# Optimization experiments

Measured on AMD Instinct MI355X. Metric: run time of the kernel, lower is better.

The kernel has to match this reference:

```python
import jax, jax.numpy as jnp
import numpy as np

WIN = 8          # current_window
PRETRAIN = 8     # pretrain_window
HEADS = 8
SHIFT = WIN // 2 # shift_size, shift_dir = [1, 1] (shift_mode=1)
L = WIN * WIN
LOG100 = float(np.log(100.0))


def _shift_mask(H, W):
    # bands (shift_dir=[1,1], no padding). Pairs from different regions get -100.
    hr = np.repeat(np.arange(3), [H - WIN, WIN - SHIFT, SHIFT])
    wr = np.repeat(np.arange(3), [W - WIN, WIN - SHIFT, SHIFT])
    region = hr[:, None] * 3 + wr[None, :]                      # [H, W]
    reg = region.reshape(H // WIN, WIN, W // WIN, WIN)
    reg = reg.transpose(0, 2, 1, 3).reshape(-1, L)              # [nw, L]
    m = np.where(reg[:, :, None] != reg[:, None, :], -100.0, 0.0)
    return jnp.asarray(m, dtype=jnp.float32)[None, :, None]     # [1, nw, 1, L, L]


def _rel_bias(cpb_w1, cpb_b1, cpb_w2):
    # Swin-v2 continuous relative position bias (log-spaced coords + MLP).
    pos = np.stack(np.meshgrid(np.arange(WIN), np.arange(WIN), indexing='ij'), -1).reshape(L, 2)
    rc = (pos[:, None, :] - pos[None, :, :]).astype(np.float32)  # [L, L, 2]
    rc = rc / (PRETRAIN - 1) * 8.0
    rc = np.sign(rc) * np.log2(np.abs(rc) + 1.0) / np.log2(8.0)
    rc = jnp.asarray(rc)
    bias = jax.nn.relu(rc @ cpb_w1 + cpb_b1) @ cpb_w2            # [L, L, heads]
    bias = 16.0 * jax.nn.sigmoid(bias)
    return bias.transpose(2, 0, 1)                               # [heads, L, L]


def _l2n(a):
    # tf.math.l2_normalize with epsilon=1.55e-5
    return a * jax.lax.rsqrt(jnp.maximum(jnp.sum(a * a, -1, keepdims=True), 1.55e-5))


def setup_inputs() -> dict:
    key = jax.random.key(0)
    ks = jax.random.split(key, 6)
    B, H, W, C = 16, 128, 128, 256
    cpb = 512
    return {
        'x': jax.random.normal(ks[0], (B, H, W, C), jnp.float32),
        'qkv_w': jax.random.normal(ks[1], (C, 3 * C), jnp.float32) * 0.02,
        'q_bias': jnp.zeros((C,), jnp.float32),
        'v_bias': jnp.zeros((C,), jnp.float32),
        'scale': jnp.full((HEADS, 1, 1), np.log(10.0), jnp.float32),
        'cpb_w1': jax.random.normal(ks[2], (2, cpb), jnp.float32) * 0.02,
        'cpb_b1': jnp.zeros((cpb,), jnp.float32),
        'cpb_w2': jax.random.normal(ks[3], (cpb, HEADS), jnp.float32) * 0.02,
        'proj_w': jax.random.normal(ks[4], (C, C), jnp.float32) * 0.02,
        'proj_b': jnp.zeros((C,), jnp.float32),
    }


def reference(x, qkv_w, q_bias, v_bias, scale, cpb_w1, cpb_b1, cpb_w2, proj_w, proj_b):
    B, H, W, C = x.shape
    units = C // HEADS
    # qkv 1x1 conv + (q, 0, v) bias
    bias = jnp.concatenate([q_bias, jnp.zeros_like(q_bias), v_bias])
    qkv = jnp.einsum('bhwc,cd->bhwd', x, qkv_w) + bias
    # cyclic shift (H, W > window so shift is applied; no padding needed)
    qkv = jnp.roll(qkv, (-SHIFT, -SHIFT), axis=(1, 2))
    # fused window partition -> [B, nw, heads, L, 3*units]
    nh, nw = H // WIN, W // WIN
    t = qkv.reshape(B, nh, WIN, nw, WIN, HEADS, 3 * units)
    t = t.transpose(0, 1, 3, 5, 2, 4, 6).reshape(B, nh * nw, HEADS, L, 3 * units)
    q, k, v = jnp.split(t, 3, axis=-1)
    # cosine attention with clamped learned logit scale
    logit_scale = jnp.exp(jnp.minimum(scale, LOG100))            # [heads, 1, 1]
    attn = jnp.einsum('bnhld,bnhmd->bnhlm', _l2n(q) * logit_scale, _l2n(k))
    attn = attn + _rel_bias(cpb_w1, cpb_b1, cpb_w2)[None, None] + _shift_mask(H, W)
    attn = jax.nn.softmax(attn, axis=-1)
    out = jnp.einsum('bnhlm,bnhmd->bnhld', attn, v)
    # reverse partition, reverse shift, output projection
    out = out.reshape(B, nh, nw, HEADS, WIN, WIN, units)
    out = out.transpose(0, 1, 4, 2, 5, 3, 6).reshape(B, H, W, C)
    out = jnp.roll(out, (SHIFT, SHIFT), axis=(1, 2))
    return jnp.einsum('bhwc,cd->bhwd', out, proj_w) + proj_b
```

## Files before the change

kernel.cpp:

```cpp
#include <hip/hip_runtime.h>

typedef __attribute__((ext_vector_type(4))) float  f32x4;
typedef __attribute__((ext_vector_type(8))) __bf16 bf16x8;
typedef __attribute__((ext_vector_type(4))) __bf16 bf16x4;

__global__ __launch_bounds__(256) void wprep_kernel(const float* __restrict__ qw,
                                                    const float* __restrict__ pw,
                                                    const float* __restrict__ qb,
                                                    const float* __restrict__ vb,
                                                    __bf16* __restrict__ W2,
                                                    __bf16* __restrict__ pT,
                                                    float* __restrict__ bcat) {
  int i = blockIdx.x * 256 + threadIdx.x;
  if (i < 24576) {
    int h = i / 3072, rem = i - h * 3072;
    int ft = rem >> 9, rem2 = rem & 511;
    int ks = rem2 >> 6, l = rem2 & 63;
    int g = l >> 4, c = l & 15;
    int col = h * 96 + ft * 16 + c;
    bf16x8 v;
    #pragma unroll
    for (int j = 0; j < 8; ++j)
      v[j] = (__bf16)qw[(ks * 32 + g * 8 + j) * 768 + col];
    *(bf16x8*)(W2 + (size_t)i * 8) = v;
  } else if (i < 24576 + 65536) {
    int j = i - 24576;
    int n = j >> 8, k = j & 255;
    pT[j] = (__bf16)pw[k * 256 + n];
  } else if (i < 24576 + 65536 + 768) {
    int cdx = i - 24576 - 65536;
    bcat[cdx] = (cdx < 256) ? qb[cdx] : ((cdx < 512) ? 0.0f : vb[cdx - 512]);
  }
}

__global__ __launch_bounds__(256) void cpb_kernel(const float* __restrict__ w1,
                                                  const float* __restrict__ b1,
                                                  const float* __restrict__ w2,
                                                  float* __restrict__ bias) {
  int pair = blockIdx.x * 256 + threadIdx.x;
  int lq = pair >> 6, mk = pair & 63;
  float d0 = (float)((lq >> 3) - (mk >> 3));
  float d1 = (float)((lq & 7) - (mk & 7));
  float v0 = d0 * (8.0f / 7.0f);
  float v1 = d1 * (8.0f / 7.0f);
  float s0 = (v0 > 0.f) ? 1.f : ((v0 < 0.f) ? -1.f : 0.f);
  float s1 = (v1 > 0.f) ? 1.f : ((v1 < 0.f) ? -1.f : 0.f);
  float r0 = s0 * log2f(fabsf(v0) + 1.0f) * (1.0f / 3.0f);
  float r1 = s1 * log2f(fabsf(v1) + 1.0f) * (1.0f / 3.0f);
  float acc[8] = {0.f, 0.f, 0.f, 0.f, 0.f, 0.f, 0.f, 0.f};
  #pragma unroll 4
  for (int j = 0; j < 512; ++j) {
    float h = fmaxf(r0 * w1[j] + r1 * w1[512 + j] + b1[j], 0.0f);
    #pragma unroll
    for (int q = 0; q < 8; ++q) acc[q] += h * w2[j * 8 + q];
  }
  #pragma unroll
  for (int q = 0; q < 8; ++q) {
    float s = 16.0f / (1.0f + __expf(-acc[q]));
    bias[(q * 64 + lq) * 64 + mk] = s;
  }
}

__device__ __forceinline__ int win_region(int tok, int wi, int wj) {
  int r = tok >> 3, cc = tok & 7;
  int rh = (wi == 15) ? ((r < 4) ? 1 : 2) : 0;
  int rw = (wj == 15) ? ((cc < 4) ? 1 : 2) : 0;
  return rh * 3 + rw;
}

__global__ __launch_bounds__(512, 2) void fused_kernel(
    const float* __restrict__ x, const __bf16* __restrict__ W2,
    const float* __restrict__ bcat, const float* __restrict__ scale,
    const float* __restrict__ cpb, __bf16* __restrict__ out)
{
  __shared__ __align__(16) __bf16 xs[64 * 256];
  __shared__ __align__(16) __bf16 qkp[8][64 * 72];
  __shared__ __align__(16) __bf16 vst[8][64 * 36];
  const f32x4 zz = {0.f, 0.f, 0.f, 0.f};

  int t = threadIdx.x;
  int h = t >> 6, l = t & 63, g = l >> 4, c = l & 15;
  int win = blockIdx.x, b = blockIdx.y;
  int wi = win >> 4, wj = win & 15;
  bool edge = (wi == 15) || (wj == 15);

  {
    int r = t >> 3;
    int q8 = t & 7;
    int ht = (wi * 8 + (r >> 3) + 4) & 127;
    int wt = (wj * 8 + (r & 7) + 4) & 127;
    const float* src = x + (size_t)((b * 128 + ht) * 128 + wt) * 256 + q8 * 32;
    #pragma unroll
    for (int q = 0; q < 4; ++q) {
      f32x4 a0 = *(const f32x4*)(src + q * 8);
      f32x4 a1 = *(const f32x4*)(src + q * 8 + 4);
      bf16x8 v;
      #pragma unroll
      for (int j = 0; j < 4; ++j) { v[j] = (__bf16)a0[j]; v[4 + j] = (__bf16)a1[j]; }
      int phys = (q8 * 4 + q) ^ (r & 7);
      *(bf16x8*)&xs[r * 256 + phys * 8] = v;
    }
  }
  __syncthreads();

  int toko[4];
  #pragma unroll
  for (int i = 0; i < 4; ++i) {
    int tok = 16 * i + c;
    int ht = (wi * 8 + (tok >> 3) + 4) & 127;
    int wt = (wj * 8 + (tok & 7) + 4) & 127;
    toko[i] = ((b * 128 + ht) * 128 + wt) * 256;
  }

  f32x4 acc[6][4];
  #pragma unroll
  for (int ft = 0; ft < 6; ++ft)
    #pragma unroll
    for (int tt = 0; tt < 4; ++tt) acc[ft][tt] = zz;

  const __bf16* Wh = W2 + (size_t)h * 24576;
  #pragma unroll
  for (int ks = 0; ks < 8; ++ks) {
    bf16x8 wf[6], xf[4];
    #pragma unroll
    for (int ft = 0; ft < 6; ++ft)
      wf[ft] = *(const bf16x8*)(Wh + (size_t)((ft * 8 + ks) * 64 + l) * 8);
    #pragma unroll
    for (int tt = 0; tt < 4; ++tt) {
      int phys = (ks * 4 + g) ^ (c & 7);
      xf[tt] = *(const bf16x8*)&xs[(tt * 16 + c) * 256 + phys * 8];
    }
    #pragma unroll
    for (int ft = 0; ft < 6; ++ft)
      #pragma unroll
      for (int tt = 0; tt < 4; ++tt)
        acc[ft][tt] = __builtin_amdgcn_mfma_f32_16x16x32_bf16(wf[ft], xf[tt], acc[ft][tt], 0, 0, 0);
  }

  #pragma unroll
  for (int ft = 0; ft < 6; ++ft) {
    f32x4 bb = *(const f32x4*)&bcat[h * 96 + ft * 16 + 4 * g];
    #pragma unroll
    for (int tt = 0; tt < 4; ++tt) acc[ft][tt] += bb;
  }

  float ls = __expf(fminf(scale[h], 4.6051701859880914f));

  #pragma unroll
  for (int tt = 0; tt < 4; ++tt) {
    float sq = 0.f, sk = 0.f;
    #pragma unroll
    for (int i = 0; i < 4; ++i) {
      sq += acc[0][tt][i] * acc[0][tt][i] + acc[1][tt][i] * acc[1][tt][i];
      sk += acc[2][tt][i] * acc[2][tt][i] + acc[3][tt][i] * acc[3][tt][i];
    }
    sq += __shfl_xor(sq, 16); sq += __shfl_xor(sq, 32);
    sk += __shfl_xor(sk, 16); sk += __shfl_xor(sk, 32);
    float rq = rsqrtf(fmaxf(sq, 1.55e-5f)) * ls;
    float rk = rsqrtf(fmaxf(sk, 1.55e-5f));
    __bf16* row = &qkp[h][(tt * 16 + c) * 72];
    bf16x4 w0, w1, w2, w3, v0, v1;
    #pragma unroll
    for (int i = 0; i < 4; ++i) {
      w0[i] = (__bf16)(acc[0][tt][i] * rq);
      w1[i] = (__bf16)(acc[1][tt][i] * rq);
      w2[i] = (__bf16)(acc[2][tt][i] * rk);
      w3[i] = (__bf16)(acc[3][tt][i] * rk);
      v0[i] = (__bf16)acc[4][tt][i];
      v1[i] = (__bf16)acc[5][tt][i];
    }
    *(bf16x4*)&row[4 * g]      = w0;
    *(bf16x4*)&row[16 + 4 * g] = w1;
    *(bf16x4*)&row[32 + 4 * g] = w2;
    *(bf16x4*)&row[48 + 4 * g] = w3;
    __bf16* vrow = &vst[h][(tt * 16 + c) * 36];
    *(bf16x4*)&vrow[4 * g]      = v0;
    *(bf16x4*)&vrow[16 + 4 * g] = v1;
  }

  bf16x8 kf[4], qf[4];
  #pragma unroll
  for (int i = 0; i < 4; ++i) {
    kf[i] = *(const bf16x8*)&qkp[h][(16 * i + c) * 72 + 32 + 8 * g];
    qf[i] = *(const bf16x8*)&qkp[h][(16 * i + c) * 72 + 8 * g];
  }

  float rsum[4];
  __bf16* Pw = &qkp[h][0];
  #pragma unroll
  for (int nt = 0; nt < 4; ++nt) {
    f32x4 tt4[4];
    #pragma unroll
    for (int mt = 0; mt < 4; ++mt)
      tt4[mt] = __builtin_amdgcn_mfma_f32_16x16x32_bf16(kf[mt], qf[nt], zz, 0, 0, 0);
    int q = nt * 16 + c;
    float p[16];
    #pragma unroll
    for (int mt = 0; mt < 4; ++mt) {
      f32x4 bb = *(const f32x4*)&cpb[(h * 64 + q) * 64 + mt * 16 + 4 * g];
      #pragma unroll
      for (int i = 0; i < 4; ++i) p[mt * 4 + i] = tt4[mt][i] + bb[i];
    }
    if (edge) {
      int regq = win_region(q, wi, wj);
      #pragma unroll
      for (int mt = 0; mt < 4; ++mt)
        #pragma unroll
        for (int i = 0; i < 4; ++i) {
          int k = mt * 16 + 4 * g + i;
          if (win_region(k, wi, wj) != regq) p[mt * 4 + i] -= 100.0f;
        }
    }
    float mx = -1e30f;
    #pragma unroll
    for (int j = 0; j < 16; ++j) mx = fmaxf(mx, p[j]);
    mx = fmaxf(mx, __shfl_xor(mx, 16));
    mx = fmaxf(mx, __shfl_xor(mx, 32));
    float sum = 0.f;
    #pragma unroll
    for (int j = 0; j < 16; ++j) { p[j] = __expf(p[j] - mx); sum += p[j]; }
    sum += __shfl_xor(sum, 16); sum += __shfl_xor(sum, 32);
    rsum[nt] = sum;
    #pragma unroll
    for (int mt = 0; mt < 4; ++mt) {
      bf16x4 px = { (__bf16)p[mt * 4 + 0], (__bf16)p[mt * 4 + 1],
                    (__bf16)p[mt * 4 + 2], (__bf16)p[mt * 4 + 3] };
      *(bf16x4*)&Pw[q * 72 + mt * 16 + 4 * g] = px;
    }
  }

  #pragma unroll
  for (int mh = 0; mh < 2; ++mh) {
    f32x4 oacc[4];
    #pragma unroll
    for (int nt = 0; nt < 4; ++nt) oacc[nt] = zz;
    #pragma unroll
    for (int ks = 0; ks < 2; ++ks) {
      bf16x8 va;
      #pragma unroll
      for (int j = 0; j < 8; ++j)
        va[j] = vst[h][(32 * ks + 8 * g + j) * 36 + 16 * mh + c];
      #pragma unroll
      for (int nt = 0; nt < 4; ++nt) {
        bf16x8 pfr = *(const bf16x8*)&Pw[(nt * 16 + c) * 72 + 32 * ks + 8 * g];
        oacc[nt] = __builtin_amdgcn_mfma_f32_16x16x32_bf16(va, pfr, oacc[nt], 0, 0, 0);
      }
    }
    #pragma unroll
    for (int nt = 0; nt < 4; ++nt) {
      float rinv = 1.0f / rsum[nt];
      bf16x4 ov = { (__bf16)(oacc[nt][0] * rinv), (__bf16)(oacc[nt][1] * rinv),
                    (__bf16)(oacc[nt][2] * rinv), (__bf16)(oacc[nt][3] * rinv) };
      *(bf16x4*)(out + toko[nt] + h * 32 + 16 * mh + 4 * g) = ov;
    }
  }
}

__global__ __launch_bounds__(256) void proj_kernel(
    const __bf16* __restrict__ A, const __bf16* __restrict__ BT,
    float* __restrict__ Cout, const float* __restrict__ pb)
{
  const int K = 256, N = 256, NB = 2;
  __shared__ __align__(16) __bf16 lA[128 * 64];
  __shared__ __align__(16) __bf16 lB[128 * 64];
  int t = threadIdx.x;
  int wv = t >> 6, l = t & 63;
  int g = l >> 4, c = l & 15;
  int wr = wv >> 1, wc = wv & 1;

  int cpx = gridDim.x >> 3;
  int lin = (blockIdx.x & 7) * cpx + (blockIdx.x >> 3);
  int mblk = lin / NB;
  int nblk = lin - mblk * NB;

  int srow = wv * 8 + (l >> 3);
  const __bf16* Ab = A + (size_t)mblk * 128 * K;
  const __bf16* Bb = BT + (size_t)nblk * 128 * K;

  f32x4 acc[4][4];
  #pragma unroll
  for (int i = 0; i < 4; ++i)
    #pragma unroll
    for (int j = 0; j < 4; ++j) acc[i][j] = (f32x4){0.f, 0.f, 0.f, 0.f};

  for (int kt = 0; kt < 4; ++kt) {
    bf16x8 ra[4], rb[4];
    #pragma unroll
    for (int p = 0; p < 4; ++p) {
      ra[p] = *(const bf16x8*)(Ab + (size_t)(p * 32 + srow) * K + kt * 64 + (l & 7) * 8);
      rb[p] = *(const bf16x8*)(Bb + (size_t)(p * 32 + srow) * K + kt * 64 + (l & 7) * 8);
    }
    __syncthreads();
    #pragma unroll
    for (int p = 0; p < 4; ++p) {
      int row = p * 32 + srow;
      int phys = (l & 7) ^ (row & 7);
      *(bf16x8*)&lA[row * 64 + phys * 8] = ra[p];
      *(bf16x8*)&lB[row * 64 + phys * 8] = rb[p];
    }
    __syncthreads();
    #pragma unroll
    for (int kk = 0; kk < 2; ++kk) {
      bf16x8 af[4], bfr[4];
      #pragma unroll
      for (int mt = 0; mt < 4; ++mt) {
        int row = wr * 64 + mt * 16 + c;
        int ch = ((kk << 2) | g) ^ (c & 7);
        af[mt] = *(const bf16x8*)&lA[row * 64 + ch * 8];
      }
      #pragma unroll
      for (int nt = 0; nt < 4; ++nt) {
        int row = wc * 64 + nt * 16 + c;
        int ch = ((kk << 2) | g) ^ (c & 7);
        bfr[nt] = *(const bf16x8*)&lB[row * 64 + ch * 8];
      }
      #pragma unroll
      for (int mt = 0; mt < 4; ++mt)
        #pragma unroll
        for (int nt = 0; nt < 4; ++nt)
          acc[mt][nt] = __builtin_amdgcn_mfma_f32_16x16x32_bf16(af[mt], bfr[nt], acc[mt][nt], 0, 0, 0);
    }
  }

  #pragma unroll
  for (int mt = 0; mt < 4; ++mt) {
    #pragma unroll
    for (int nt = 0; nt < 4; ++nt) {
      int row0 = mblk * 128 + wr * 64 + mt * 16 + 4 * g;
      int col  = nblk * 128 + wc * 64 + nt * 16 + c;
      float bias = pb[col];
      #pragma unroll
      for (int i = 0; i < 4; ++i)
        Cout[(size_t)(row0 + i) * N + col] = acc[mt][nt][i] + bias;
    }
  }
}

extern "C" void kernel_launch(void* const* d_in, const int* in_sizes, int n_in,
                              void* d_out, int out_size, void* d_ws, size_t ws_size,
                              hipStream_t stream)
{
  const float* x      = (const float*)d_in[0];
  const float* qkv_w  = (const float*)d_in[1];
  const float* q_bias = (const float*)d_in[2];
  const float* v_bias = (const float*)d_in[3];
  const float* scale  = (const float*)d_in[4];
  const float* cpb_w1 = (const float*)d_in[5];
  const float* cpb_b1 = (const float*)d_in[6];
  const float* cpb_w2 = (const float*)d_in[7];
  const float* proj_w = (const float*)d_in[8];
  const float* proj_b = (const float*)d_in[9];

  char* ws = (char*)d_ws;
  __bf16* aout = (__bf16*)(ws);
  __bf16* W2   = (__bf16*)(ws + 134217728LL);
  __bf16* pT   = (__bf16*)(ws + 134610944LL);
  float*  bcat = (float*) (ws + 134742016LL);
  float*  cpb  = (float*) (ws + 134745088LL);

  wprep_kernel<<<355, 256, 0, stream>>>(qkv_w, proj_w, q_bias, v_bias, W2, pT, bcat);
  cpb_kernel<<<16, 256, 0, stream>>>(cpb_w1, cpb_b1, cpb_w2, cpb);
  fused_kernel<<<dim3(256, 16), 512, 0, stream>>>(x, W2, bcat, scale, cpb, aout);
  proj_kernel<<<4096, 256, 0, stream>>>(aout, pT, (float*)d_out, proj_b);
}
```

Before: 407.0 us.

## Fuse output projection into windowed attention kernel via shared-memory staging

Removes the separate projection GEMM kernel. Each block writes its attention output back into the xs shared buffer with a swizzled layout, then every wave computes a 32-column slice of the output projection with MFMA and writes fp32 results straight to the destination. This drops the 128 MB bf16 intermediate round trip through global memory and one kernel launch. It adds extra MFMA work and more register pressure to the already heavy fused kernel, plus an extra barrier.

```diff
diff --git a/kernel.cpp b/kernel.cpp
--- a/kernel.cpp
+++ b/kernel.cpp
@@ -9,7 +9,7 @@
                                                     const float* __restrict__ qb,
                                                     const float* __restrict__ vb,
                                                     __bf16* __restrict__ W2,
-                                                    __bf16* __restrict__ pT,
+                                                    __bf16* __restrict__ Wp,
                                                     float* __restrict__ bcat) {
   int i = blockIdx.x * 256 + threadIdx.x;
   if (i < 24576) {
@@ -23,12 +23,20 @@
     for (int j = 0; j < 8; ++j)
       v[j] = (__bf16)qw[(ks * 32 + g * 8 + j) * 768 + col];
     *(bf16x8*)(W2 + (size_t)i * 8) = v;
-  } else if (i < 24576 + 65536) {
+  } else if (i < 24576 + 8192) {
     int j = i - 24576;
-    int n = j >> 8, k = j & 255;
-    pT[j] = (__bf16)pw[k * 256 + n];
-  } else if (i < 24576 + 65536 + 768) {
-    int cdx = i - 24576 - 65536;
+    int wv = j >> 10, rem = j & 1023;
+    int ft = rem >> 9, rem2 = rem & 511;
+    int ks = rem2 >> 6, l = rem2 & 63;
+    int g = l >> 4, c = l & 15;
+    int col = wv * 32 + ft * 16 + c;
+    bf16x8 v;
+    #pragma unroll
+    for (int j8 = 0; j8 < 8; ++j8)
+      v[j8] = (__bf16)pw[(ks * 32 + g * 8 + j8) * 256 + col];
+    *(bf16x8*)(Wp + (size_t)j * 8) = v;
+  } else if (i < 24576 + 8192 + 768) {
+    int cdx = i - 24576 - 8192;
     bcat[cdx] = (cdx < 256) ? qb[cdx] : ((cdx < 512) ? 0.0f : vb[cdx - 512]);
   }
 }
@@ -70,8 +78,9 @@
 
 __global__ __launch_bounds__(512, 2) void fused_kernel(
     const float* __restrict__ x, const __bf16* __restrict__ W2,
-    const float* __restrict__ bcat, const float* __restrict__ scale,
-    const float* __restrict__ cpb, __bf16* __restrict__ out)
+    const __bf16* __restrict__ Wp, const float* __restrict__ bcat,
+    const float* __restrict__ scale, const float* __restrict__ cpb,
+    const float* __restrict__ pb, float* __restrict__ outf)
 {
   __shared__ __align__(16) __bf16 xs[64 * 256];
   __shared__ __align__(16) __bf16 qkp[8][64 * 72];
@@ -136,6 +145,7 @@
       for (int tt = 0; tt < 4; ++tt)
         acc[ft][tt] = __builtin_amdgcn_mfma_f32_16x16x32_bf16(wf[ft], xf[tt], acc[ft][tt], 0, 0, 0);
   }
+  __syncthreads();
 
   #pragma unroll
   for (int ft = 0; ft < 6; ++ft) {
@@ -246,92 +256,51 @@
         oacc[nt] = __builtin_amdgcn_mfma_f32_16x16x32_bf16(va, pfr, oacc[nt], 0, 0, 0);
       }
     }
+    int chunk = h * 4 + 2 * mh + (g >> 1);
     #pragma unroll
     for (int nt = 0; nt < 4; ++nt) {
       float rinv = 1.0f / rsum[nt];
+      int tok = nt * 16 + c;
+      int phys = chunk ^ (tok & 7);
       bf16x4 ov = { (__bf16)(oacc[nt][0] * rinv), (__bf16)(oacc[nt][1] * rinv),
                     (__bf16)(oacc[nt][2] * rinv), (__bf16)(oacc[nt][3] * rinv) };
-      *(bf16x4*)(out + toko[nt] + h * 32 + 16 * mh + 4 * g) = ov;
-    }
-  }
-}
-
-__global__ __launch_bounds__(256) void proj_kernel(
-    const __bf16* __restrict__ A, const __bf16* __restrict__ BT,
-    float* __restrict__ Cout, const float* __restrict__ pb)
-{
-  const int K = 256, N = 256, NB = 2;
-  __shared__ __align__(16) __bf16 lA[128 * 64];
-  __shared__ __align__(16) __bf16 lB[128 * 64];
-  int t = threadIdx.x;
-  int wv = t >> 6, l = t & 63;
-  int g = l >> 4, c = l & 15;
-  int wr = wv >> 1, wc = wv & 1;
-
-  int cpx = gridDim.x >> 3;
-  int lin = (blockIdx.x & 7) * cpx + (blockIdx.x >> 3);
-  int mblk = lin / NB;
-  int nblk = lin - mblk * NB;
-
-  int srow = wv * 8 + (l >> 3);
-  const __bf16* Ab = A + (size_t)mblk * 128 * K;
-  const __bf16* Bb = BT + (size_t)nblk * 128 * K;
-
-  f32x4 acc[4][4];
-  #pragma unroll
-  for (int i = 0; i < 4; ++i)
-    #pragma unroll
-    for (int j = 0; j < 4; ++j) acc[i][j] = (f32x4){0.f, 0.f, 0.f, 0.f};
-
-  for (int kt = 0; kt < 4; ++kt) {
-    bf16x8 ra[4], rb[4];
-    #pragma unroll
-    for (int p = 0; p < 4; ++p) {
-      ra[p] = *(const bf16x8*)(Ab + (size_t)(p * 32 + srow) * K + kt * 64 + (l & 7) * 8);
-      rb[p] = *(const bf16x8*)(Bb + (size_t)(p * 32 + srow) * K + kt * 64 + (l & 7) * 8);
-    }
-    __syncthreads();
-    #pragma unroll
-    for (int p = 0; p < 4; ++p) {
-      int row = p * 32 + srow;
-      int phys = (l & 7) ^ (row & 7);
-      *(bf16x8*)&lA[row * 64 + phys * 8] = ra[p];
-      *(bf16x8*)&lB[row * 64 + phys * 8] = rb[p];
-    }
-    __syncthreads();
-    #pragma unroll
-    for (int kk = 0; kk < 2; ++kk) {
-      bf16x8 af[4], bfr[4];
-      #pragma unroll
-      for (int mt = 0; mt < 4; ++mt) {
-        int row = wr * 64 + mt * 16 + c;
-        int ch = ((kk << 2) | g) ^ (c & 7);
-        af[mt] = *(const bf16x8*)&lA[row * 64 + ch * 8];
-      }
-      #pragma unroll
-      for (int nt = 0; nt < 4; ++nt) {
-        int row = wc * 64 + nt * 16 + c;
-        int ch = ((kk << 2) | g) ^ (c & 7);
-        bfr[nt] = *(const bf16x8*)&lB[row * 64 + ch * 8];
-      }
-      #pragma unroll
-      for (int mt = 0; mt < 4; ++mt)
-        #pragma unroll
-        for (int nt = 0; nt < 4; ++nt)
-          acc[mt][nt] = __builtin_amdgcn_mfma_f32_16x16x32_bf16(af[mt], bfr[nt], acc[mt][nt], 0, 0, 0);
-    }
-  }
-
-  #pragma unroll
-  for (int mt = 0; mt < 4; ++mt) {
-    #pragma unroll
-    for (int nt = 0; nt < 4; ++nt) {
-      int row0 = mblk * 128 + wr * 64 + mt * 16 + 4 * g;
-      int col  = nblk * 128 + wc * 64 + nt * 16 + c;
-      float bias = pb[col];
-      #pragma unroll
-      for (int i = 0; i < 4; ++i)
-        Cout[(size_t)(row0 + i) * N + col] = acc[mt][nt][i] + bias;
+      *(bf16x4*)&xs[tok * 256 + phys * 8 + 4 * (g & 1)] = ov;
+    }
+  }
+  __syncthreads();
+
+  f32x4 acc2[2][4];
+  #pragma unroll
+  for (int ft = 0; ft < 2; ++ft)
+    #pragma unroll
+    for (int tt = 0; tt < 4; ++tt) acc2[ft][tt] = zz;
+
+  const __bf16* Wph = Wp + (size_t)h * 8192;
+  #pragma unroll
+  for (int ks = 0; ks < 8; ++ks) {
+    bf16x8 wf[2], xf[4];
+    #pragma unroll
+    for (int ft = 0; ft < 2; ++ft)
+      wf[ft] = *(const bf16x8*)(Wph + (size_t)((ft * 8 + ks) * 64 + l) * 8);
+    #pragma unroll
+    for (int tt = 0; tt < 4; ++tt) {
+      int phys = (ks * 4 + g) ^ (c & 7);
+      xf[tt] = *(const bf16x8*)&xs[(tt * 16 + c) * 256 + phys * 8];
+    }
+    #pragma unroll
+    for (int ft = 0; ft < 2; ++ft)
+      #pragma unroll
+      for (int tt = 0; tt < 4; ++tt)
+        acc2[ft][tt] = __builtin_amdgcn_mfma_f32_16x16x32_bf16(wf[ft], xf[tt], acc2[ft][tt], 0, 0, 0);
+  }
+
+  #pragma unroll
+  for (int ft = 0; ft < 2; ++ft) {
+    f32x4 bb = *(const f32x4*)&pb[h * 32 + ft * 16 + 4 * g];
+    #pragma unroll
+    for (int tt = 0; tt < 4; ++tt) {
+      f32x4 res = acc2[ft][tt] + bb;
+      *(f32x4*)&outf[toko[tt] + h * 32 + ft * 16 + 4 * g] = res;
     }
   }
 }
@@ -352,14 +321,13 @@
   const float* proj_b = (const float*)d_in[9];
 
   char* ws = (char*)d_ws;
-  __bf16* aout = (__bf16*)(ws);
-  __bf16* W2   = (__bf16*)(ws + 134217728LL);
-  __bf16* pT   = (__bf16*)(ws + 134610944LL);
-  float*  bcat = (float*) (ws + 134742016LL);
-  float*  cpb  = (float*) (ws + 134745088LL);
-
-  wprep_kernel<<<355, 256, 0, stream>>>(qkv_w, proj_w, q_bias, v_bias, W2, pT, bcat);
+  __bf16* W2   = (__bf16*)(ws);
+  __bf16* Wp   = (__bf16*)(ws + 393216LL);
+  float*  bcat = (float*) (ws + 524288LL);
+  float*  cpb  = (float*) (ws + 527360LL);
+
+  wprep_kernel<<<131, 256, 0, stream>>>(qkv_w, proj_w, q_bias, v_bias, W2, Wp, bcat);
   cpb_kernel<<<16, 256, 0, stream>>>(cpb_w1, cpb_b1, cpb_w2, cpb);
-  fused_kernel<<<dim3(256, 16), 512, 0, stream>>>(x, W2, bcat, scale, cpb, aout);
-  proj_kernel<<<4096, 256, 0, stream>>>(aout, pT, (float*)d_out, proj_b);
-}
+  fused_kernel<<<dim3(256, 16), 512, 0, stream>>>(x, W2, Wp, bcat, scale, cpb,
+                                                  proj_b, (float*)d_out);
+}
```

Measured after the change: 430.4 us. 1.06x slower.
